# Kernel tuning notes

Measured on AMD Instinct MI355X. Metric: run time of the kernel, lower is better.

## Reference

```python
import jax, jax.numpy as jnp
import numpy as np

EMBED_DIM = 1024


def setup_inputs() -> dict:
    key = jax.random.key(0)
    kx, kq, kk = jax.random.split(key, 3)
    x = jax.random.normal(kx, (4, 4096, EMBED_DIM), dtype=jnp.float32)
    Wq = jax.random.normal(kq, (EMBED_DIM, EMBED_DIM), dtype=jnp.float32)
    Wk = jax.random.normal(kk, (EMBED_DIM, EMBED_DIM), dtype=jnp.float32)
    return {"x": x, "Wq": Wq, "Wk": Wk}


def reference(x, Wq, Wk):
    # q, k projections; v is the raw input (as in the source module)
    q = jnp.einsum('bse,ef->bsf', x, Wq)
    k = jnp.einsum('bse,ef->bsf', x, Wk)
    scale = 1.0 / np.sqrt(EMBED_DIM).astype(np.float32)
    # full [B, S, S] score matrix, softmax over last (key) axis
    scores = jax.nn.softmax(jnp.einsum('bqd,bkd->bqk', q, k) * scale, axis=-1)
    return jnp.einsum('bqk,bkd->bqd', scores, x)
```

## Files before the change

kernel.cpp:

```cpp
#include <hip/hip_runtime.h>
#include <stdint.h>

typedef __attribute__((ext_vector_type(8))) short v8s;
typedef __attribute__((ext_vector_type(4))) short v4s;
typedef __attribute__((ext_vector_type(4))) float v4f;

#define MFMA(a, b, c) __builtin_amdgcn_mfma_f32_16x16x32_bf16((a), (b), (c), 0, 0, 0)

__device__ __forceinline__ unsigned short f2bf(float f) {
    unsigned int u = __float_as_uint(f);
    u += 0x7fffu + ((u >> 16) & 1u);
    return (unsigned short)(u >> 16);
}
__device__ __forceinline__ float bf2f(unsigned short h) {
    return __uint_as_float(((unsigned int)h) << 16);
}
__device__ __forceinline__ unsigned int fkey(float f) {
    unsigned int u = __float_as_uint(f);
    return (u & 0x80000000u) ? ~u : (u | 0x80000000u);
}
__device__ __forceinline__ float kinv(unsigned int k) {
    unsigned int u = (k & 0x80000000u) ? (k & 0x7FFFFFFFu) : ~k;
    return __uint_as_float(u);
}

__device__ __forceinline__ void gload16(const void* g, void* l) {
    __builtin_amdgcn_global_load_lds((const __attribute__((address_space(1))) void*)g,
                                     (__attribute__((address_space(3))) void*)l, 16, 0, 0);
}

#define NB 4
#define SEQ 4096
#define ED 1024
#define CAND_CAP 256

#define XHI_OFF   (0ll)
#define XLO_OFF   (33554432ll)
#define YHI_OFF   (67108864ll)
#define YLO_OFF   (100663296ll)
#define CNT_OFF   (134217728ll)
#define RMX_OFF   (134283264ll)
#define LIST_OFF  (134348800ll)
#define WQH_OFF   (167903232ll)
#define WQL_OFF   (170000384ll)
#define WKH_OFF   (172097536ll)
#define WKL_OFF   (174194688ll)
#define MTH_OFF   (176291840ll)
#define MTL_OFF   (178388992ll)
#define WS_NEED   (180486144ll)

__global__ __launch_bounds__(256) void prep_x(const float* __restrict__ x,
                                              unsigned short* __restrict__ xhi,
                                              unsigned short* __restrict__ xlo) {
    long idx = ((long)blockIdx.x * 256 + threadIdx.x) * 4;
    v4f v = *(const v4f*)(x + idx);
    v4s ph, pl;
#pragma unroll
    for (int e = 0; e < 4; ++e) {
        unsigned short hi = f2bf(v[e]);
        ph[e] = (short)hi;
        pl[e] = (short)f2bf(v[e] - bf2f(hi));
    }
    *(v4s*)(xhi + idx) = ph;
    *(v4s*)(xlo + idx) = pl;
}

__global__ __launch_bounds__(256) void prep_w2(const float* __restrict__ wq,
                                               const float* __restrict__ wk,
                                               unsigned short* __restrict__ wqh,
                                               unsigned short* __restrict__ wql,
                                               unsigned short* __restrict__ wkh,
                                               unsigned short* __restrict__ wkl) {
    const float* w = blockIdx.z ? wk : wq;
    unsigned short* oh = blockIdx.z ? wkh : wqh;
    unsigned short* ol = blockIdx.z ? wkl : wql;
    long idx = ((long)blockIdx.x * 256 + threadIdx.x) * 4;
    v4f v = *(const v4f*)(w + idx);
    v4s ph, pl;
#pragma unroll
    for (int e = 0; e < 4; ++e) {
        unsigned short hi = f2bf(v[e]);
        ph[e] = (short)hi;
        pl[e] = (short)f2bf(v[e] - bf2f(hi));
    }
    *(v4s*)(oh + idx) = ph;
    *(v4s*)(ol + idx) = pl;
}

__global__ __launch_bounds__(256) void init_cand(unsigned int* __restrict__ cnt,
                                                 unsigned int* __restrict__ rmx) {
    int i = blockIdx.x * 256 + threadIdx.x;
    cnt[i] = 0u;
    rmx[i] = 0u;
}

__global__ __launch_bounds__(256, 2) void gemm_m(const unsigned short* __restrict__ ah,
                                                 const unsigned short* __restrict__ al,
                                                 const unsigned short* __restrict__ bh,
                                                 const unsigned short* __restrict__ bl,
                                                 unsigned short* __restrict__ ch,
                                                 unsigned short* __restrict__ cl) {
    __shared__ __align__(16) unsigned char lds[65536];
    int m0 = blockIdx.x * 128, n0 = blockIdx.y * 128;
    int tid = threadIdx.x, lane = tid & 63, wave = tid >> 6;
    int mo = (wave & 1) * 64, no = (wave >> 1) * 64;
    int lr = lane >> 3;
    int scol = (((lane & 7) ^ lr) << 4);
    v4f vzero = {0.f, 0.f, 0.f, 0.f};
    v4f acc[4][4];
#pragma unroll
    for (int i = 0; i < 4; ++i)
#pragma unroll
        for (int j = 0; j < 4; ++j) acc[i][j] = vzero;
    int cb0 = 16 * (lane >> 4);

    for (int ks = 0; ks < 16; ++ks) {
        __syncthreads();
#pragma unroll
        for (int j = 0; j < 4; ++j) {
            int c = j * 4 + wave;
            int row = c * 8 + lr;
            long ga = ((long)(m0 + row) * ED + ks * 64) * 2 + scol;
            long gb = ((long)(n0 + row) * ED + ks * 64) * 2 + scol;
            unsigned loff = c * 1024;
            gload16((const unsigned char*)ah + ga, lds + loff);
            gload16((const unsigned char*)al + ga, lds + 16384 + loff);
            gload16((const unsigned char*)bh + gb, lds + 32768 + loff);
            gload16((const unsigned char*)bl + gb, lds + 49152 + loff);
        }
        __syncthreads();
#pragma unroll
        for (int kk = 0; kk < 2; ++kk) {
            v8s fah[4], fal[4], fbh[4], fbl[4];
#pragma unroll
            for (int i = 0; i < 4; ++i) {
                int ra = mo + i * 16 + (lane & 15);
                int ca = (kk * 64 + cb0) ^ ((ra & 7) << 4);
                fah[i] = *(const v8s*)(lds +         ra * 128 + ca);
                fal[i] = *(const v8s*)(lds + 16384 + ra * 128 + ca);
                int rb = no + i * 16 + (lane & 15);
                int cbb = (kk * 64 + cb0) ^ ((rb & 7) << 4);
                fbh[i] = *(const v8s*)(lds + 32768 + rb * 128 + cbb);
                fbl[i] = *(const v8s*)(lds + 49152 + rb * 128 + cbb);
            }
#pragma unroll
            for (int i = 0; i < 4; ++i)
#pragma unroll
                for (int j = 0; j < 4; ++j) {
                    acc[i][j] = MFMA(fah[i], fbh[j], acc[i][j]);
                    acc[i][j] = MFMA(fah[i], fbl[j], acc[i][j]);
                    acc[i][j] = MFMA(fal[i], fbh[j], acc[i][j]);
                    acc[i][j] = MFMA(fal[i], fbl[j], acc[i][j]);
                }
        }
    }
#pragma unroll
    for (int i = 0; i < 4; ++i)
#pragma unroll
        for (int j = 0; j < 4; ++j)
#pragma unroll
            for (int r = 0; r < 4; ++r) {
                int row = m0 + mo + i * 16 + (lane >> 4) * 4 + r;
                int col = n0 + no + j * 16 + (lane & 15);
                float v = acc[i][j][r];
                unsigned short hi = f2bf(v);
                long o = (long)row * ED + col;
                ch[o] = hi;
                cl[o] = f2bf(v - bf2f(hi));
            }
}

__global__ __launch_bounds__(256, 2) void gemm_y(const unsigned short* __restrict__ ah,
                                                 const unsigned short* __restrict__ al,
                                                 const unsigned short* __restrict__ bh,
                                                 const unsigned short* __restrict__ bl,
                                                 unsigned short* __restrict__ ch,
                                                 unsigned short* __restrict__ cl) {
    __shared__ __align__(16) unsigned char lds[65536];
    int m0 = blockIdx.x * 128, n0 = blockIdx.y * 128;
    int tid = threadIdx.x, lane = tid & 63, wave = tid >> 6;
    int mo = (wave & 1) * 64, no = (wave >> 1) * 64;
    int lr = lane >> 3;
    int scol = (((lane & 7) ^ lr) << 4);
    v4f vzero = {0.f, 0.f, 0.f, 0.f};
    v4f acc[4][4];
#pragma unroll
    for (int i = 0; i < 4; ++i)
#pragma unroll
        for (int j = 0; j < 4; ++j) acc[i][j] = vzero;
    int cb0 = 16 * (lane >> 4);

    for (int ks = 0; ks < 16; ++ks) {
        __syncthreads();
#pragma unroll
        for (int j = 0; j < 4; ++j) {
            int c = j * 4 + wave;
            int row = c * 8 + lr;
            long ga = ((long)(m0 + row) * ED + ks * 64) * 2 + scol;
            long gb = ((long)(n0 + row) * ED + ks * 64) * 2 + scol;
            unsigned loff = c * 1024;
            gload16((const unsigned char*)ah + ga, lds + loff);
            gload16((const unsigned char*)al + ga, lds + 16384 + loff);
            gload16((const unsigned char*)bh + gb, lds + 32768 + loff);
            gload16((const unsigned char*)bl + gb, lds + 49152 + loff);
        }
        __syncthreads();
#pragma unroll
        for (int kk = 0; kk < 2; ++kk) {
            v8s fah[4], fal[4], fbh[4], fbl[4];
#pragma unroll
            for (int i = 0; i < 4; ++i) {
                int ra = mo + i * 16 + (lane & 15);
                int ca = (kk * 64 + cb0) ^ ((ra & 7) << 4);
                fah[i] = *(const v8s*)(lds +         ra * 128 + ca);
                fal[i] = *(const v8s*)(lds + 16384 + ra * 128 + ca);
                int rb = no + i * 16 + (lane & 15);
                int cbb = (kk * 64 + cb0) ^ ((rb & 7) << 4);
                fbh[i] = *(const v8s*)(lds + 32768 + rb * 128 + cbb);
                fbl[i] = *(const v8s*)(lds + 49152 + rb * 128 + cbb);
            }
#pragma unroll
            for (int i = 0; i < 4; ++i)
#pragma unroll
                for (int j = 0; j < 4; ++j) {
                    acc[i][j] = MFMA(fah[i], fbh[j], acc[i][j]);
                    acc[i][j] = MFMA(fah[i], fbl[j], acc[i][j]);
                    acc[i][j] = MFMA(fal[i], fbh[j], acc[i][j]);
                }
        }
    }
#pragma unroll
    for (int i = 0; i < 4; ++i)
#pragma unroll
        for (int j = 0; j < 4; ++j)
#pragma unroll
            for (int r = 0; r < 4; ++r) {
                int row = m0 + mo + i * 16 + (lane >> 4) * 4 + r;
                int col = n0 + no + j * 16 + (lane & 15);
                float v = acc[i][j][r];
                unsigned short hi = f2bf(v);
                long o = (long)row * ED + col;
                ch[o] = hi;
                cl[o] = f2bf(v - bf2f(hi));
            }
}

__global__ __launch_bounds__(256, 4) void gemm_cand(const unsigned short* __restrict__ qh,
                                                    const unsigned short* __restrict__ kh,
                                                    unsigned int* __restrict__ cnt,
                                                    unsigned int* __restrict__ rmx,
                                                    unsigned long long* __restrict__ list) {
    __shared__ __align__(16) unsigned char lds[32768];
    int b = blockIdx.z;
    int m0 = blockIdx.x * 128, n0 = blockIdx.y * 128;
    int tid = threadIdx.x, lane = tid & 63, wave = tid >> 6;
    int mo = (wave & 1) * 64, no = (wave >> 1) * 64;
    int lr = lane >> 3;
    int scol = (((lane & 7) ^ lr) << 4);
    v4f vzero = {0.f, 0.f, 0.f, 0.f};
    v4f acc[4][4];
#pragma unroll
    for (int i = 0; i < 4; ++i)
#pragma unroll
        for (int j = 0; j < 4; ++j) acc[i][j] = vzero;
    int cb0 = 16 * (lane >> 4);

    for (int ks = 0; ks < 16; ++ks) {
        __syncthreads();
#pragma unroll
        for (int j = 0; j < 4; ++j) {
            int c = j * 4 + wave;
            int row = c * 8 + lr;
            long ga = ((long)(b * SEQ + m0 + row) * ED + ks * 64) * 2 + scol;
            long gb = ((long)(b * SEQ + n0 + row) * ED + ks * 64) * 2 + scol;
            unsigned loff = c * 1024;
            gload16((const unsigned char*)qh + ga, lds + loff);
            gload16((const unsigned char*)kh + gb, lds + 16384 + loff);
        }
        __syncthreads();
#pragma unroll
        for (int kk = 0; kk < 2; ++kk) {
            v8s fa[4], fb[4];
#pragma unroll
            for (int i = 0; i < 4; ++i) {
                int ra = mo + i * 16 + (lane & 15);
                int ca = (kk * 64 + cb0) ^ ((ra & 7) << 4);
                fa[i] = *(const v8s*)(lds +         ra * 128 + ca);
                int rb = no + i * 16 + (lane & 15);
                int cbb = (kk * 64 + cb0) ^ ((rb & 7) << 4);
                fb[i] = *(const v8s*)(lds + 16384 + rb * 128 + cbb);
            }
#pragma unroll
            for (int i = 0; i < 4; ++i)
#pragma unroll
                for (int j = 0; j < 4; ++j)
                    acc[i][j] = MFMA(fa[i], fb[j], acc[i][j]);
        }
    }

#pragma unroll
    for (int i = 0; i < 4; ++i)
#pragma unroll
        for (int r = 0; r < 4; ++r) {
            float v = fmaxf(fmaxf(acc[i][0][r], acc[i][1][r]),
                            fmaxf(acc[i][2][r], acc[i][3][r])) * 0.03125f;
            v = fmaxf(v, __shfl_xor(v, 1));
            v = fmaxf(v, __shfl_xor(v, 2));
            v = fmaxf(v, __shfl_xor(v, 4));
            v = fmaxf(v, __shfl_xor(v, 8));
            int row = m0 + mo + i * 16 + (lane >> 4) * 4 + r;
            int gr = b * SEQ + row;
            float thr;
            if ((lane & 15) == 0) {
                unsigned int old = atomicMax(&rmx[gr], fkey(v));
                float cur = fmaxf(v, kinv(old));
                thr = cur - 60.0f;
            }
            thr = __shfl(thr, lane & 48);
#pragma unroll
            for (int j = 0; j < 4; ++j) {
                float sv = acc[i][j][r] * 0.03125f;
                if (sv > thr) {
                    unsigned int idx = atomicAdd(&cnt[gr], 1u);
                    if (idx < CAND_CAP) {
                        unsigned int col = (unsigned int)(n0 + no + j * 16 + (lane & 15));
                        list[(long)gr * CAND_CAP + idx] =
                            ((unsigned long long)fkey(sv) << 32) | col;
                    }
                }
            }
        }
}

__global__ __launch_bounds__(128) void attn_sparse(const unsigned int* __restrict__ cnt,
                                                   const unsigned long long* __restrict__ list,
                                                   const unsigned short* __restrict__ yhi,
                                                   const unsigned short* __restrict__ ylo,
                                                   const float* __restrict__ x,
                                                   float* __restrict__ out) {
    __shared__ int scnt[2];
    __shared__ int scol[2][64];
    __shared__ float pval[2][64];
    int w = threadIdx.x >> 6, lane = threadIdx.x & 63;
    int b = blockIdx.y;
    int row = blockIdx.x * 2 + w;
    int gr = b * SEQ + row;
    int n = (int)cnt[gr];
    if (n > CAND_CAP) n = CAND_CAP;
    if (lane == 0) scnt[w] = 0;

    const unsigned long long* lrow = list + (long)gr * CAND_CAP;
    unsigned int mk = 0u;
    for (int c = lane; c < n; c += 64) mk = max(mk, (unsigned int)(lrow[c] >> 32));
#pragma unroll
    for (int o = 1; o < 64; o <<= 1) {
        unsigned int other = (unsigned int)__shfl_xor((int)mk, o);
        mk = max(mk, other);
    }
    float thrf = kinv(mk) - 60.0f;

    for (int c = lane; c < n; c += 64) {
        unsigned long long e = lrow[c];
        if (kinv((unsigned int)(e >> 32)) > thrf) {
            int idx = atomicAdd(&scnt[w], 1);
            if (idx < 64) scol[w][idx] = (int)(e & 0xFFFFFFFFu);
        }
    }
    __syncthreads();
    int sn = scnt[w] < 64 ? scnt[w] : 64;

    long ybase = (long)gr * ED;
    int k0 = lane * 16;
    v8s yh0 = *(const v8s*)(yhi + ybase + k0);
    v8s yh1 = *(const v8s*)(yhi + ybase + k0 + 8);
    v8s yl0 = *(const v8s*)(ylo + ybase + k0);
    v8s yl1 = *(const v8s*)(ylo + ybase + k0 + 8);
    float yv[16];
#pragma unroll
    for (int e = 0; e < 8; ++e) {
        yv[e]     = bf2f((unsigned short)yh0[e]) + bf2f((unsigned short)yl0[e]);
        yv[8 + e] = bf2f((unsigned short)yh1[e]) + bf2f((unsigned short)yl1[e]);
    }
    float M = -INFINITY;
    for (int c = 0; c < sn; ++c) {
        const float* xr = x + ((long)b * SEQ + scol[w][c]) * ED + k0;
        float s = 0.f;
#pragma unroll
        for (int t = 0; t < 4; ++t) {
            v4f xv = *(const v4f*)(xr + t * 4);
#pragma unroll
            for (int e = 0; e < 4; ++e) s += yv[t * 4 + e] * xv[e];
        }
#pragma unroll
        for (int o = 1; o < 64; o <<= 1) s += __shfl_xor(s, o);
        s *= 0.03125f;
        if (lane == 0) pval[w][c] = s;
        M = fmaxf(M, s);
    }

    float sum = 0.f;
    for (int c = 0; c < sn; ++c) sum += __expf(pval[w][c] - M);
    float inv = 1.0f / sum;
    v4f a0 = {0.f, 0.f, 0.f, 0.f}, a1 = a0, a2 = a0, a3 = a0;
    for (int c = 0; c < sn; ++c) {
        float p = __expf(pval[w][c] - M) * inv;
        const float* xr = x + ((long)b * SEQ + scol[w][c]) * ED + k0;
        v4f x0 = *(const v4f*)(xr);
        v4f x1 = *(const v4f*)(xr + 4);
        v4f x2 = *(const v4f*)(xr + 8);
        v4f x3 = *(const v4f*)(xr + 12);
#pragma unroll
        for (int e = 0; e < 4; ++e) {
            a0[e] += p * x0[e];
            a1[e] += p * x1[e];
            a2[e] += p * x2[e];
            a3[e] += p * x3[e];
        }
    }
    float* orow = out + (long)gr * ED + k0;
    *(v4f*)(orow)      = a0;
    *(v4f*)(orow + 4)  = a1;
    *(v4f*)(orow + 8)  = a2;
    *(v4f*)(orow + 12) = a3;
}

extern "C" void kernel_launch(void* const* d_in, const int* in_sizes, int n_in,
                              void* d_out, int out_size, void* d_ws, size_t ws_size,
                              hipStream_t stream) {
    const float* x  = (const float*)d_in[0];
    const float* wq = (const float*)d_in[1];
    const float* wk = (const float*)d_in[2];
    unsigned char* ws = (unsigned char*)d_ws;
    unsigned short* xhi = (unsigned short*)(ws + XHI_OFF);
    unsigned short* xlo = (unsigned short*)(ws + XLO_OFF);
    unsigned short* yhi = (unsigned short*)(ws + YHI_OFF);
    unsigned short* ylo = (unsigned short*)(ws + YLO_OFF);
    unsigned int*   cnt = (unsigned int*)(ws + CNT_OFF);
    unsigned int*   rmx = (unsigned int*)(ws + RMX_OFF);
    unsigned long long* list = (unsigned long long*)(ws + LIST_OFF);
    unsigned short* wqh = (unsigned short*)(ws + WQH_OFF);
    unsigned short* wql = (unsigned short*)(ws + WQL_OFF);
    unsigned short* wkh = (unsigned short*)(ws + WKH_OFF);
    unsigned short* wkl = (unsigned short*)(ws + WKL_OFF);
    unsigned short* mth = (unsigned short*)(ws + MTH_OFF);
    unsigned short* mtl = (unsigned short*)(ws + MTL_OFF);

    prep_x<<<16384, 256, 0, stream>>>(x, xhi, xlo);
    prep_w2<<<dim3(1024, 1, 2), 256, 0, stream>>>(wq, wk, wqh, wql, wkh, wkl);
    init_cand<<<64, 256, 0, stream>>>(cnt, rmx);
    gemm_m<<<dim3(8, 8), 256, 0, stream>>>(wkh, wkl, wqh, wql, mth, mtl);
    gemm_y<<<dim3(128, 8), 256, 0, stream>>>(xhi, xlo, mth, mtl, yhi, ylo);
    gemm_cand<<<dim3(32, 32, NB), 256, 0, stream>>>(yhi, xhi, cnt, rmx, list);
    attn_sparse<<<dim3(SEQ / 2, NB), 128, 0, stream>>>(cnt, list, yhi, ylo, x, (float*)d_out);
}
```

Baseline: 348.1 us.

## Use FP8 e4m3 MFMA for candidate-scoring GEMM with widened threshold window

The candidate-selection GEMM (Y·Xᵀ scores) now runs on FP8 e4m3 operands with the fp8 MFMA instead of bf16, halving operand bytes and LDS footprint. Two new conversion kernels quantize x and the scaled y to FP8 in a permuted layout matching the MFMA operand order. The score scale and candidate window are adjusted (window widened to 340) to absorb the coarser FP8 error, with exact attention still computed from hi/lo bf16 data. The risk is more candidates overflowing the per-row cap and the added conversion passes costing extra memory traffic.

```diff
diff --git a/kernel.cpp b/kernel.cpp
--- a/kernel.cpp
+++ b/kernel.cpp
@@ -4,8 +4,10 @@
 typedef __attribute__((ext_vector_type(8))) short v8s;
 typedef __attribute__((ext_vector_type(4))) short v4s;
 typedef __attribute__((ext_vector_type(4))) float v4f;
+typedef __attribute__((ext_vector_type(4))) unsigned int v4u;
 
 #define MFMA(a, b, c) __builtin_amdgcn_mfma_f32_16x16x32_bf16((a), (b), (c), 0, 0, 0)
+#define MFMA8(a, b, c) __builtin_amdgcn_mfma_f32_16x16x32_fp8_fp8((a), (b), (c), 0, 0, 0)
 
 __device__ __forceinline__ unsigned short f2bf(float f) {
     unsigned int u = __float_as_uint(f);
@@ -23,6 +25,21 @@
     unsigned int u = (k & 0x80000000u) ? (k & 0x7FFFFFFFu) : ~k;
     return __uint_as_float(u);
 }
+__device__ __forceinline__ unsigned char f2e4m3(float f) {
+    unsigned int u = __float_as_uint(f);
+    unsigned int s = (u >> 24) & 0x80u;
+    float a = fabsf(f);
+    if (!(a < 448.0f)) return (unsigned char)(s | 0x7Eu);
+    if (a < 0.015625f) {
+        int mi = (int)(a * 512.0f + 0.5f);
+        return (unsigned char)(s | (unsigned int)mi);
+    }
+    unsigned int au = (u & 0x7FFFFFFFu) + 0x00080000u;
+    int e = (int)((au >> 23) & 0xFFu) - 120;
+    unsigned int m3 = (au >> 20) & 7u;
+    if (e > 15 || (e == 15 && m3 == 7u)) return (unsigned char)(s | 0x7Eu);
+    return (unsigned char)(s | ((unsigned int)e << 3) | m3);
+}
 
 __device__ __forceinline__ void gload16(const void* g, void* l) {
     __builtin_amdgcn_global_load_lds((const __attribute__((address_space(1))) void*)g,
@@ -33,6 +50,7 @@
 #define SEQ 4096
 #define ED 1024
 #define CAND_CAP 256
+#define WINDOW 340.0f
 
 #define XHI_OFF   (0ll)
 #define XLO_OFF   (33554432ll)
@@ -47,7 +65,9 @@
 #define WKL_OFF   (174194688ll)
 #define MTH_OFF   (176291840ll)
 #define MTL_OFF   (178388992ll)
-#define WS_NEED   (180486144ll)
+#define XF8_OFF   (180486144ll)
+#define YF8_OFF   (197263360ll)
+#define WS_NEED   (214040576ll)
 
 __global__ __launch_bounds__(256) void prep_x(const float* __restrict__ x,
                                               unsigned short* __restrict__ xhi,
@@ -85,6 +105,20 @@
     }
     *(v4s*)(oh + idx) = ph;
     *(v4s*)(ol + idx) = pl;
+}
+
+__global__ __launch_bounds__(256) void conv_f8(const unsigned short* __restrict__ hi,
+                                               unsigned char* __restrict__ out, float scale) {
+    long idx = (long)blockIdx.x * 256 + threadIdx.x;
+    long k0 = idx * 8;
+    v8s h = *(const v8s*)(hi + k0);
+    long pos = (k0 & ~63l) | (((k0 >> 3) & 3) << 4) | (((k0 >> 5) & 1) << 3);
+    unsigned char o[8];
+#pragma unroll
+    for (int e = 0; e < 8; ++e) o[e] = f2e4m3(bf2f((unsigned short)h[e]) * scale);
+    uint2 wv;
+    __builtin_memcpy(&wv, o, 8);
+    *(uint2*)(out + pos) = wv;
 }
 
 __global__ __launch_bounds__(256) void init_cand(unsigned int* __restrict__ cnt,
@@ -245,57 +279,57 @@
             }
 }
 
-__global__ __launch_bounds__(256, 4) void gemm_cand(const unsigned short* __restrict__ qh,
-                                                    const unsigned short* __restrict__ kh,
+__global__ __launch_bounds__(256, 4) void gemm_cand(const unsigned char* __restrict__ qf8,
+                                                    const unsigned char* __restrict__ kf8,
                                                     unsigned int* __restrict__ cnt,
                                                     unsigned int* __restrict__ rmx,
                                                     unsigned long long* __restrict__ list) {
-    __shared__ __align__(16) unsigned char lds[32768];
+    __shared__ __align__(16) unsigned char lds[16384];
     int b = blockIdx.z;
     int m0 = blockIdx.x * 128, n0 = blockIdx.y * 128;
     int tid = threadIdx.x, lane = tid & 63, wave = tid >> 6;
     int mo = (wave & 1) * 64, no = (wave >> 1) * 64;
-    int lr = lane >> 3;
-    int scol = (((lane & 7) ^ lr) << 4);
+    int rsub = lane >> 2;
+    int sslot = (((lane & 3) ^ (rsub & 3)) << 4);
+    int g = lane >> 4;
     v4f vzero = {0.f, 0.f, 0.f, 0.f};
     v4f acc[4][4];
 #pragma unroll
     for (int i = 0; i < 4; ++i)
 #pragma unroll
         for (int j = 0; j < 4; ++j) acc[i][j] = vzero;
-    int cb0 = 16 * (lane >> 4);
 
     for (int ks = 0; ks < 16; ++ks) {
         __syncthreads();
 #pragma unroll
-        for (int j = 0; j < 4; ++j) {
+        for (int j = 0; j < 2; ++j) {
             int c = j * 4 + wave;
-            int row = c * 8 + lr;
-            long ga = ((long)(b * SEQ + m0 + row) * ED + ks * 64) * 2 + scol;
-            long gb = ((long)(b * SEQ + n0 + row) * ED + ks * 64) * 2 + scol;
-            unsigned loff = c * 1024;
-            gload16((const unsigned char*)qh + ga, lds + loff);
-            gload16((const unsigned char*)kh + gb, lds + 16384 + loff);
-        }
-        __syncthreads();
-#pragma unroll
-        for (int kk = 0; kk < 2; ++kk) {
-            v8s fa[4], fb[4];
-#pragma unroll
-            for (int i = 0; i < 4; ++i) {
-                int ra = mo + i * 16 + (lane & 15);
-                int ca = (kk * 64 + cb0) ^ ((ra & 7) << 4);
-                fa[i] = *(const v8s*)(lds +         ra * 128 + ca);
-                int rb = no + i * 16 + (lane & 15);
-                int cbb = (kk * 64 + cb0) ^ ((rb & 7) << 4);
-                fb[i] = *(const v8s*)(lds + 16384 + rb * 128 + cbb);
-            }
-#pragma unroll
-            for (int i = 0; i < 4; ++i)
-#pragma unroll
-                for (int j = 0; j < 4; ++j)
-                    acc[i][j] = MFMA(fa[i], fb[j], acc[i][j]);
-        }
+            int row = c * 16 + rsub;
+            long ga = (long)(b * SEQ + m0 + row) * ED + ks * 64 + sslot;
+            long gb = (long)(b * SEQ + n0 + row) * ED + ks * 64 + sslot;
+            gload16(qf8 + ga, lds + c * 1024);
+            gload16(kf8 + gb, lds + 8192 + c * 1024);
+        }
+        __syncthreads();
+        long long a0[4], a1[4], b0[4], b1[4];
+#pragma unroll
+        for (int i = 0; i < 4; ++i) {
+            int ra = mo + i * 16 + (lane & 15);
+            v4u va = *(const v4u*)(lds + ra * 64 + ((g ^ (ra & 3)) << 4));
+            a0[i] = (long long)(((unsigned long long)va[1] << 32) | va[0]);
+            a1[i] = (long long)(((unsigned long long)va[3] << 32) | va[2]);
+            int rb = no + i * 16 + (lane & 15);
+            v4u vb = *(const v4u*)(lds + 8192 + rb * 64 + ((g ^ (rb & 3)) << 4));
+            b0[i] = (long long)(((unsigned long long)vb[1] << 32) | vb[0]);
+            b1[i] = (long long)(((unsigned long long)vb[3] << 32) | vb[2]);
+        }
+#pragma unroll
+        for (int i = 0; i < 4; ++i)
+#pragma unroll
+            for (int j = 0; j < 4; ++j) {
+                acc[i][j] = MFMA8(a0[i], b0[j], acc[i][j]);
+                acc[i][j] = MFMA8(a1[i], b1[j], acc[i][j]);
+            }
     }
 
 #pragma unroll
@@ -303,7 +337,7 @@
 #pragma unroll
         for (int r = 0; r < 4; ++r) {
             float v = fmaxf(fmaxf(acc[i][0][r], acc[i][1][r]),
-                            fmaxf(acc[i][2][r], acc[i][3][r])) * 0.03125f;
+                            fmaxf(acc[i][2][r], acc[i][3][r])) * 0.5f;
             v = fmaxf(v, __shfl_xor(v, 1));
             v = fmaxf(v, __shfl_xor(v, 2));
             v = fmaxf(v, __shfl_xor(v, 4));
@@ -314,12 +348,12 @@
             if ((lane & 15) == 0) {
                 unsigned int old = atomicMax(&rmx[gr], fkey(v));
                 float cur = fmaxf(v, kinv(old));
-                thr = cur - 60.0f;
+                thr = cur - WINDOW;
             }
             thr = __shfl(thr, lane & 48);
 #pragma unroll
             for (int j = 0; j < 4; ++j) {
-                float sv = acc[i][j][r] * 0.03125f;
+                float sv = acc[i][j][r] * 0.5f;
                 if (sv > thr) {
                     unsigned int idx = atomicAdd(&cnt[gr], 1u);
                     if (idx < CAND_CAP) {
@@ -357,7 +391,7 @@
         unsigned int other = (unsigned int)__shfl_xor((int)mk, o);
         mk = max(mk, other);
     }
-    float thrf = kinv(mk) - 60.0f;
+    float thrf = kinv(mk) - WINDOW;
 
     for (int c = lane; c < n; c += 64) {
         unsigned long long e = lrow[c];
@@ -444,12 +478,16 @@
     unsigned short* wkl = (unsigned short*)(ws + WKL_OFF);
     unsigned short* mth = (unsigned short*)(ws + MTH_OFF);
     unsigned short* mtl = (unsigned short*)(ws + MTL_OFF);
+    unsigned char*  xf8 = (unsigned char*)(ws + XF8_OFF);
+    unsigned char*  yf8 = (unsigned char*)(ws + YF8_OFF);
 
     prep_x<<<16384, 256, 0, stream>>>(x, xhi, xlo);
     prep_w2<<<dim3(1024, 1, 2), 256, 0, stream>>>(wq, wk, wqh, wql, wkh, wkl);
     init_cand<<<64, 256, 0, stream>>>(cnt, rmx);
+    conv_f8<<<8192, 256, 0, stream>>>(xhi, xf8, 1.0f);
     gemm_m<<<dim3(8, 8), 256, 0, stream>>>(wkh, wkl, wqh, wql, mth, mtl);
     gemm_y<<<dim3(128, 8), 256, 0, stream>>>(xhi, xlo, mth, mtl, yhi, ylo);
-    gemm_cand<<<dim3(32, 32, NB), 256, 0, stream>>>(yhi, xhi, cnt, rmx, list);
+    conv_f8<<<8192, 256, 0, stream>>>(yhi, yf8, 0.0625f);
+    gemm_cand<<<dim3(32, 32, NB), 256, 0, stream>>>(yf8, xf8, cnt, rmx, list);
     attn_sparse<<<dim3(SEQ / 2, NB), 128, 0, stream>>>(cnt, list, yhi, ylo, x, (float*)d_out);
 }
```

New measurement: 388.2 us. 11.5% more time.
